# Optimization experiments

Hardware: AMD Instinct MI355X
Metric: run time of the kernel (lower is better)

The kernel has to match this reference:

```python
import jax, jax.numpy as jnp
import numpy as np

B, T_MAX, H, O, M, F = 256, 512, 512, 128, 512, 256


def setup_inputs() -> dict:
    key = jax.random.key(0)
    ks = jax.random.split(key, 20)
    s = 0.05
    n = lambda k, shape: (jax.random.normal(k, shape, dtype=jnp.float32) * s)
    features = jax.random.normal(ks[0], (B, F), dtype=jnp.float32)
    # PackedSequence-style: lengths sorted descending
    lengths = jnp.sort(jax.random.randint(ks[1], (B,), 1, T_MAX + 1))[::-1].astype(jnp.int32)
    return {
        'features': features,
        'lengths': lengths,
        'W_f2h': n(ks[2], (2 * H, F)), 'b_f2h': n(ks[3], (2 * H,)),
        'W_ih': n(ks[4], (4 * H, O)), 'W_hh': n(ks[5], (4 * H, H)),
        'b_ih': n(ks[6], (4 * H,)), 'b_hh': n(ks[7], (4 * H,)),
        'p1_W1': n(ks[8], (M, H)), 'p1_b1': n(ks[9], (M,)),
        'p1_W2': n(ks[10], (O, M)), 'p1_b2': n(ks[11], (O,)),
        'p2_W1': n(ks[12], (M, H)), 'p2_b1': n(ks[13], (M,)),
        'p2_W2': n(ks[14], (O, M)), 'p2_b2': n(ks[15], (O,)),
        'oW1': n(ks[16], (M, H)), 'ob1': n(ks[17], (M,)),
        'oW2': n(ks[18], (1, M)), 'ob2': n(ks[19], (1,)),
    }


def _mlp(x, W1, b1, W2, b2):
    return jnp.tanh(x @ W1.T + b1) @ W2.T + b2


def _packed_indices(lengths_np):
    T = int(lengths_np.max())
    bs = (lengths_np[None, :] > np.arange(T)[:, None]).sum(1)  # shrinking batch sizes
    t_idx = np.repeat(np.arange(T), bs)
    b_idx = np.concatenate([np.arange(n) for n in bs])
    return T, t_idx, b_idx


def reference(features, lengths, W_f2h, b_f2h, W_ih, W_hh, b_ih, b_hh,
              p1_W1, p1_b1, p1_W2, p1_b2, p2_W1, p2_b1, p2_W2, p2_b2,
              oW1, ob1, oW2, ob2):
    T, t_idx, b_idx = _packed_indices(np.asarray(lengths))

    # feature2hidden + view(-1, H, 2) split into (h, c)
    hc = (features @ W_f2h.T + b_f2h).reshape(-1, H, 2)
    h0, c0 = hc[..., 0], hc[..., 1]

    def step(carry, _):
        x, h, c = carry
        gates = x @ W_ih.T + b_ih + h @ W_hh.T + b_hh  # [B, 4H]
        i, f, g, o = jnp.split(gates, 4, axis=-1)
        c = jax.nn.sigmoid(f) * c + jax.nn.sigmoid(i) * jnp.tanh(g)
        h = jax.nn.sigmoid(o) * jnp.tanh(c)
        p1 = _mlp(h, p1_W1, p1_b1, p1_W2, p1_b2)
        p2 = _mlp(h, p2_W1, p2_b1, p2_W2, p2_b2)
        # emission_sampler in mean mode: next input = param1
        return (p1, h, c), (h, p1, p2)

    x0 = jnp.zeros((features.shape[0], O), dtype=features.dtype)
    _, (hs, p1s, p2s) = jax.lax.scan(step, (x0, h0, c0), None, length=T)

    # gather packed (flattened) outputs; rows >= batch_size[t] are never emitted,
    # matching the torch shrinking-batch loop exactly
    rnn_flat = hs[t_idx, b_idx]
    p1_flat = p1s[t_idx, b_idx]
    p2_flat = p2s[t_idx, b_idx]
    out_flat = p1_flat  # batched_input = emission_sampler(p1, p2) = p1
    offset_flat = _mlp(rnn_flat, oW1, ob1, oW2, ob2)[..., 0]
    return ((p1_flat, p2_flat), offset_flat, out_flat)
```

## Files before the change

kernel.cpp:

```cpp
#include <hip/hip_runtime.h>
#include <hip/hip_bf16.h>


#define NBLK 256
#define NTHR 512
#define ACT_STRIDE 2096

typedef __attribute__((ext_vector_type(8))) short bf16x8;
typedef __attribute__((ext_vector_type(4))) float f32x4;
typedef __hip_bfloat16 bf16;
typedef unsigned long long u64;

#define WS_BAR     0ull
#define WS_BS      32768ull
#define WS_OFF     34816ull
#define WS_BIASQ0  36864ull
#define WS_BIASQF  45056ull
#define WS_BCAT    53248ull
#define WS_B2CAT   59392ull
#define WS_C0      61440ull
#define WS_H       585728ull
#define WS_ACAT    1110016ull
#define WS_WQF     2682880ull
#define WS_W1T     6877184ull
#define WS_W2T     8450048ull

#define LDSG_OFF   67072
#define DYN_LDS    84480

__device__ __forceinline__ float sigm(float x) { return 1.0f / (1.0f + __expf(-x)); }
__device__ __forceinline__ unsigned short f2bu(float x) {
  bf16 b = __float2bfloat16(x);
  return *(unsigned short*)&b;
}
__device__ __forceinline__ u64 ld8a(const void* p) {
  return __hip_atomic_load((const u64*)p, __ATOMIC_RELAXED, __HIP_MEMORY_SCOPE_AGENT);
}
__device__ __forceinline__ bf16x8 ld16a(const short* p) {
  union { u64 u[2]; bf16x8 v; } t;
  t.u[0] = ld8a(p);
  t.u[1] = ld8a(p + 4);
  return t.v;
}
__device__ __forceinline__ void st4c(short* p, unsigned v) {
  __hip_atomic_store((unsigned*)p, v, __ATOMIC_RELAXED, __HIP_MEMORY_SCOPE_AGENT);
}
__device__ __forceinline__ bf16x8 actA(const char* smem, int row, int k0) {
  return *(const bf16x8*)(smem + row * ACT_STRIDE + k0 * 2);
}

__global__ void k_fold(char* ws, const float* __restrict__ Wih, const float* __restrict__ Whh,
                       const float* __restrict__ bih, const float* __restrict__ bhh,
                       const float* __restrict__ p1W2, const float* __restrict__ p1b2) {
  const int q = blockIdx.x;
  const int j = q >> 2, g = q & 3;
  const int orig = g * 512 + j;
  __shared__ float wih[128];
  if (threadIdx.x < 128) wih[threadIdx.x] = Wih[orig * 128 + threadIdx.x];
  __syncthreads();
  bf16* Wq = (bf16*)(ws + WS_WQF);
  for (int k = threadIdx.x; k < 512; k += 256)
    Wq[(size_t)q * 1024 + k] = __float2bfloat16(Whh[orig * 512 + k]);
  for (int m = threadIdx.x; m < 512; m += 256) {
    float s = 0.f;
    for (int o = 0; o < 128; ++o) s += wih[o] * p1W2[o * 512 + m];
    Wq[(size_t)q * 1024 + 512 + m] = __float2bfloat16(s);
  }
  if (threadIdx.x == 0) {
    float b0 = bih[orig] + bhh[orig];
    ((float*)(ws + WS_BIASQ0))[q] = b0;
    float s = 0.f;
    for (int o = 0; o < 128; ++o) s += wih[o] * p1b2[o];
    ((float*)(ws + WS_BIASQF))[q] = b0 + s;
  }
}

__global__ void k_w1t(char* ws, const float* w1a, const float* b1a, const float* w1b,
                      const float* b1b, const float* w1c, const float* b1c) {
  const int r = blockIdx.x;
  const int m = r & 511;
  const float* src = (r < 512) ? w1a : ((r < 1024) ? w1b : w1c);
  const float* bsrc = (r < 512) ? b1a : ((r < 1024) ? b1b : b1c);
  bf16* W = (bf16*)(ws + WS_W1T);
  const int c16 = r >> 4, l15 = r & 15;
  for (int k = threadIdx.x; k < 512; k += 256) {
    const int kk = k >> 5, l16 = (k >> 3) & 3, jj = k & 7;
    const size_t dst = ((((size_t)c16 * 16 + kk) * 16 + l15) * 4 + l16) * 8 + jj;
    W[dst] = __float2bfloat16(src[m * 512 + k]);
  }
  if (threadIdx.x == 0) ((float*)(ws + WS_BCAT))[r] = bsrc[m];
}

__global__ void k_w2t(char* ws, const float* w2a, const float* b2a, const float* w2b,
                      const float* b2b, const float* w2c, const float* b2c) {
  const int r = blockIdx.x;
  bf16* W = (bf16*)(ws + WS_W2T);
  float* bb = (float*)(ws + WS_B2CAT);
  const float* src = nullptr; const float* bsrc = nullptr; int m = 0;
  if (r < 128)      { src = w2a; bsrc = b2a; m = r; }
  else if (r < 256) { src = w2b; bsrc = b2b; m = r - 128; }
  else if (r == 256){ src = w2c; bsrc = b2c; m = 0; }
  const int t16 = r >> 4, l15 = r & 15;
  for (int k = threadIdx.x; k < 512; k += 256) {
    const int kk = k >> 5, l16 = (k >> 3) & 3, jj = k & 7;
    const size_t dst = ((((size_t)t16 * 16 + kk) * 16 + l15) * 4 + l16) * 8 + jj;
    W[dst] = src ? __float2bfloat16(src[m * 512 + k]) : __float2bfloat16(0.f);
  }
  if (threadIdx.x == 0) bb[r] = src ? bsrc[m] : 0.f;
}

__global__ void k_h0c0(char* ws, const float* __restrict__ features,
                       const float* __restrict__ Wf2h, const float* __restrict__ bf2h_) {
  const int r = blockIdx.x;
  __shared__ float feat[256];
  feat[threadIdx.x] = features[r * 256 + threadIdx.x];
  __syncthreads();
  float* C0 = (float*)(ws + WS_C0);
  bf16* H0 = (bf16*)(ws + WS_H);
  for (int n = threadIdx.x; n < 1024; n += 256) {
    float s = bf2h_[n];
    for (int k = 0; k < 256; ++k) s += Wf2h[n * 256 + k] * feat[k];
    const int j = n >> 1;
    if (n & 1) C0[r * 512 + j] = s;
    else       H0[(size_t)r * 512 + j] = __float2bfloat16(s);
  }
}

__global__ void k_bs(char* ws, const int* __restrict__ lengths) {
  __shared__ int sl[256];
  __shared__ int sbs[512];
  const int t = threadIdx.x;
  if (t < 256) sl[t] = lengths[t];
  __syncthreads();
  int c = 0;
  for (int b = 0; b < 256; ++b) c += (sl[b] > t) ? 1 : 0;
  sbs[t] = c;
  ((int*)(ws + WS_BS))[t] = c;
  __syncthreads();
  int o = 0;
  for (int u = 0; u < t; ++u) o += sbs[u];
  ((int*)(ws + WS_OFF))[t] = o;
}

__device__ __forceinline__ void stage_tile(char* smem, const short* gsrc, int rowstride,
                                           int R0, int ofs, int tid) {
  u64 v[8];
#pragma unroll
  for (int it = 0; it < 8; ++it) {
    const int c = tid + it * 512;
    const int row = c >> 7, cc = c & 127;
    v[it] = ld8a(gsrc + (size_t)(R0 + row) * rowstride + cc * 4);
  }
#pragma unroll
  for (int it = 0; it < 8; ++it) {
    const int c = tid + it * 512;
    const int row = c >> 7, cc = c & 127;
    *(u64*)(smem + row * ACT_STRIDE + ofs + cc * 8) = v[it];
  }
}

__device__ __forceinline__ void do_outs(int tm1, const short* __restrict__ Acur, int R0,
                                        int rt2, int l15, int l16, int tile,
                                        const short* __restrict__ W2T, const float* __restrict__ b2cat,
                                        const int* __restrict__ bsarr, const int* __restrict__ offarr,
                                        float* __restrict__ out, int N) {
  const int kb = tile < 8 ? 0 : (tile < 16 ? 512 : 1024);
  const short* ar = Acur + (size_t)(R0 + rt2 * 16 + l15) * 1536 + kb + l16 * 8;
  f32x4 acc = {0.f, 0.f, 0.f, 0.f};
#pragma unroll
  for (int kk = 0; kk < 16; ++kk) {
    bf16x8 av = ld16a(ar + kk * 32);
    bf16x8 bv = *(const bf16x8*)(W2T + ((((size_t)tile * 16 + kk) * 16 + l15) * 4 + l16) * 8);
    acc = __builtin_amdgcn_mfma_f32_16x16x32_bf16(av, bv, acc, 0, 0, 0);
  }
  const int wrow = tile * 16 + l15;
  const float bb = b2cat[wrow];
  const int bsz = bsarr[tm1], base = offarr[tm1];
  const int col = wrow;
  float* out_p1 = out;
  float* out_p2 = out + (size_t)N * 128;
  float* out_of = out + (size_t)N * 256;
  float* out_xx = out + (size_t)N * 257;
#pragma unroll
  for (int r = 0; r < 4; ++r) {
    const int R = R0 + rt2 * 16 + l16 * 4 + r;
    if (R < bsz) {
      const float v = acc[r] + bb;
      const size_t orow = (size_t)(base + R);
      if (col < 128)      { out_p1[orow * 128 + col] = v; out_xx[orow * 128 + col] = v; }
      else if (col < 256) { out_p2[orow * 128 + col - 128] = v; }
      else if (l15 == 0)  { out_of[orow] = v; }
    }
  }
}

__global__ void __launch_bounds__(NTHR) scan_kernel(char* ws, const int* __restrict__ lengths,
                                                    float* __restrict__ out, int N) {
  extern __shared__ char smem[];
  float* ldsg = (float*)(smem + LDSG_OFF);

  const int bid = blockIdx.x, tid = threadIdx.x;
  const int grp = bid >> 5, lb = bid & 31;
  const int R0 = grp * 32;
  const int wave = tid >> 6, lane = tid & 63;
  const int l15 = lane & 15, l16 = lane >> 4;

  unsigned* barG = (unsigned*)(ws + WS_BAR) + grp * 1024;
  const int* bsarr = (const int*)(ws + WS_BS);
  const int* offarr = (const int*)(ws + WS_OFF);
  const float* biasq0 = (const float*)(ws + WS_BIASQ0);
  const float* biasqF = (const float*)(ws + WS_BIASQF);
  const float* bcat = (const float*)(ws + WS_BCAT);
  const float* b2cat = (const float*)(ws + WS_B2CAT);
  const float* C0 = (const float*)(ws + WS_C0);
  short* Hb = (short*)(ws + WS_H);
  short* Ab = (short*)(ws + WS_ACAT);
  const short* WQF = (const short*)(ws + WS_WQF);
  const short* W1T = (const short*)(ws + WS_W1T);
  const short* W2T = (const short*)(ws + WS_W2T);

  const int ct = wave & 3, khalf = wave >> 2;
  const int qb = lb * 64;
  const int ct3 = (wave < 6) ? (wave % 3) : 0;
  const int rt3 = (wave < 6) ? (wave / 3) : 0;
  const int cb = lb * 48 + ct3 * 16;

  stage_tile(smem, Hb, 512, R0, 0, tid);

  bf16x8 bfrA[16];
#pragma unroll
  for (int kk = 0; kk < 16; ++kk)
    bfrA[kk] = *(const bf16x8*)(WQF + (size_t)(qb + ct * 16 + l15) * 1024 +
                                khalf * 512 + kk * 32 + l16 * 8);
  bf16x8 bfrB[16];
  if (wave < 6) {
    const int cb16 = lb * 3 + ct3;
#pragma unroll
    for (int kk = 0; kk < 16; ++kk)
      bfrB[kk] = *(const bf16x8*)(W1T + ((((size_t)cb16 * 16 + kk) * 16 + l15) * 4 + l16) * 8);
  }
  const float bbB = (wave < 6) ? bcat[cb + l15] : 0.f;

  const int Lr = tid >> 4, lj = tid & 15;
  float c_reg = C0[(R0 + Lr) * 512 + lb * 16 + lj];
  float b0_[4], bF_[4];
#pragma unroll
  for (int g = 0; g < 4; ++g) {
    const int q = qb + lj * 4 + g;
    b0_[g] = biasq0[q];
    bF_[g] = biasqF[q];
  }
  const int Lg = lengths[R0];
  __syncthreads();

  for (int t = 0; t < Lg; ++t) {
    const int par = t & 1, parn = par ^ 1;

    f32x4 acc0 = {0.f, 0.f, 0.f, 0.f}, acc1 = {0.f, 0.f, 0.f, 0.f};
    if (!(t == 0 && khalf == 1)) {
#pragma unroll
      for (int kk = 0; kk < 16; ++kk) {
        const int k0 = khalf * 512 + kk * 32 + l16 * 8;
        bf16x8 a0 = actA(smem, l15, k0);
        bf16x8 a1v = actA(smem, 16 + l15, k0);
        acc0 = __builtin_amdgcn_mfma_f32_16x16x32_bf16(a0, bfrA[kk], acc0, 0, 0, 0);
        acc1 = __builtin_amdgcn_mfma_f32_16x16x32_bf16(a1v, bfrA[kk], acc1, 0, 0, 0);
      }
    }
    {
      float* lg = ldsg + khalf * 2176;
#pragma unroll
      for (int r = 0; r < 4; ++r) {
        lg[(l16 * 4 + r) * 68 + ct * 16 + l15] = acc0[r];
        lg[(16 + l16 * 4 + r) * 68 + ct * 16 + l15] = acc1[r];
      }
    }
    __syncthreads();

    {
      const float* g0 = ldsg + Lr * 68 + lj * 4;
      const float* g1 = ldsg + 2176 + Lr * 68 + lj * 4;
      const float gi = g0[0] + g1[0] + (t ? bF_[0] : b0_[0]);
      const float gf = g0[1] + g1[1] + (t ? bF_[1] : b0_[1]);
      const float gg = g0[2] + g1[2] + (t ? bF_[2] : b0_[2]);
      const float go = g0[3] + g1[3] + (t ? bF_[3] : b0_[3]);
      c_reg = sigm(gf) * c_reg + sigm(gi) * tanhf(gg);
      const float h = sigm(go) * tanhf(c_reg);
      const float hp = __shfl_xor(h, 1);
      if ((lj & 1) == 0) {
        const unsigned v = (unsigned)f2bu(h) | ((unsigned)f2bu(hp) << 16);
        st4c(Hb + parn * (256 * 512) + (size_t)(R0 + Lr) * 512 + lb * 16 + lj, v);
      }
    }

    __syncthreads();
    if (tid == 0) {
      __hip_atomic_fetch_add(&barG[t * 2], 1u, __ATOMIC_RELAXED, __HIP_MEMORY_SCOPE_AGENT);
      while (__hip_atomic_load(&barG[t * 2], __ATOMIC_RELAXED, __HIP_MEMORY_SCOPE_AGENT) < 32u)
        __builtin_amdgcn_s_sleep(1);
    }
    __syncthreads();

    stage_tile(smem, Hb + parn * (256 * 512), 512, R0, 0, tid);
    __syncthreads();

    if (wave < 6) {
      f32x4 a3 = {0.f, 0.f, 0.f, 0.f};
#pragma unroll
      for (int kk = 0; kk < 16; ++kk) {
        bf16x8 av = actA(smem, rt3 * 16 + l15, kk * 32 + l16 * 8);
        a3 = __builtin_amdgcn_mfma_f32_16x16x32_bf16(av, bfrB[kk], a3, 0, 0, 0);
      }
      short* aout = Ab + parn * (256 * 1536);
#pragma unroll
      for (int r = 0; r < 4; ++r) {
        const float v = tanhf(a3[r] + bbB);
        const float vp = __shfl_xor(v, 1);
        if ((l15 & 1) == 0) {
          const unsigned pv = (unsigned)f2bu(v) | ((unsigned)f2bu(vp) << 16);
          st4c(aout + (size_t)(R0 + rt3 * 16 + l16 * 4 + r) * 1536 + cb + l15, pv);
        }
      }
    } else if (t > 0 && lb < 17) {
      do_outs(t - 1, Ab + par * (256 * 1536), R0, wave - 6, l15, l16, lb, W2T, b2cat,
              bsarr, offarr, out, N);
    }

    __syncthreads();
    if (tid == 0) {
      __hip_atomic_fetch_add(&barG[t * 2 + 1], 1u, __ATOMIC_RELAXED, __HIP_MEMORY_SCOPE_AGENT);
      while (__hip_atomic_load(&barG[t * 2 + 1], __ATOMIC_RELAXED, __HIP_MEMORY_SCOPE_AGENT) < 32u)
        __builtin_amdgcn_s_sleep(1);
    }
    __syncthreads();

    stage_tile(smem, Ab + parn * (256 * 1536), 1536, R0, 1024, tid);
    __syncthreads();
  }

  if (lb < 17 && wave >= 6)
    do_outs(Lg - 1, Ab + (Lg & 1) * (256 * 1536), R0, wave - 6, l15, l16, lb, W2T, b2cat,
            bsarr, offarr, out, N);
}

extern "C" void kernel_launch(void* const* d_in, const int* in_sizes, int n_in,
                              void* d_out, int out_size, void* d_ws, size_t ws_size,
                              hipStream_t stream) {
  const float* features = (const float*)d_in[0];
  const int* lengths = (const int*)d_in[1];
  const float* Wf2h = (const float*)d_in[2];
  const float* bf2h_ = (const float*)d_in[3];
  const float* Wih = (const float*)d_in[4];
  const float* Whh = (const float*)d_in[5];
  const float* bih = (const float*)d_in[6];
  const float* bhh = (const float*)d_in[7];
  const float* p1W1 = (const float*)d_in[8];
  const float* p1b1 = (const float*)d_in[9];
  const float* p1W2 = (const float*)d_in[10];
  const float* p1b2 = (const float*)d_in[11];
  const float* p2W1 = (const float*)d_in[12];
  const float* p2b1 = (const float*)d_in[13];
  const float* p2W2 = (const float*)d_in[14];
  const float* p2b2 = (const float*)d_in[15];
  const float* oW1 = (const float*)d_in[16];
  const float* ob1 = (const float*)d_in[17];
  const float* oW2 = (const float*)d_in[18];
  const float* ob2 = (const float*)d_in[19];

  char* ws = (char*)d_ws;
  float* outp = (float*)d_out;
  int N = out_size / 385;

  hipMemsetAsync(ws + WS_BAR, 0, 32768, stream);
  k_fold<<<2048, 256, 0, stream>>>(ws, Wih, Whh, bih, bhh, p1W2, p1b2);
  k_w1t<<<1536, 256, 0, stream>>>(ws, p1W1, p1b1, p2W1, p2b1, oW1, ob1);
  k_w2t<<<272, 256, 0, stream>>>(ws, p1W2, p1b2, p2W2, p2b2, oW2, ob2);
  k_h0c0<<<256, 256, 0, stream>>>(ws, features, Wf2h, bf2h_);
  k_bs<<<1, 512, 0, stream>>>(ws, lengths);

  hipFuncSetAttribute((const void*)scan_kernel,
                      hipFuncAttributeMaxDynamicSharedMemorySize, DYN_LDS);

  const int* lenv = lengths;
  void* args[] = {&ws, &lenv, &outp, &N};
  hipLaunchCooperativeKernel((const void*)scan_kernel, dim3(NBLK), dim3(NTHR),
                             args, DYN_LDS, stream);
}
```

Baseline: 6.227 ms.

## Restructure LSTM scan step to overlap MLP hidden layer with recurrent GEMM

Reorganizes each time step so the recurrent h·W_hh part of the gates and the MLP hidden-layer GEMM (h·W1, tanh) run concurrently on different waves from the same staged h tile. The folded p1-input contribution is then computed after a grid barrier from the freshly staged A tile. This removes one serial phase from the per-step critical path. The output projection (do_outs) now runs between the barrier arrive and wait, so it is overlapped with the barrier latency. Barrier counters double in size and an epilogue step handles the final hidden layer, adding extra complexity around the barrier indexing.

```diff
diff --git a/kernel.cpp b/kernel.cpp
--- a/kernel.cpp
+++ b/kernel.cpp
@@ -12,18 +12,18 @@
 typedef unsigned long long u64;
 
 #define WS_BAR     0ull
-#define WS_BS      32768ull
-#define WS_OFF     34816ull
-#define WS_BIASQ0  36864ull
-#define WS_BIASQF  45056ull
-#define WS_BCAT    53248ull
-#define WS_B2CAT   59392ull
-#define WS_C0      61440ull
-#define WS_H       585728ull
-#define WS_ACAT    1110016ull
-#define WS_WQF     2682880ull
-#define WS_W1T     6877184ull
-#define WS_W2T     8450048ull
+#define WS_BS      65536ull
+#define WS_OFF     67584ull
+#define WS_BIASQ0  69632ull
+#define WS_BIASQF  77824ull
+#define WS_BCAT    86016ull
+#define WS_B2CAT   92160ull
+#define WS_C0      94208ull
+#define WS_H       618496ull
+#define WS_ACAT    1142784ull
+#define WS_WQF     2715648ull
+#define WS_W1T     6909952ull
+#define WS_W2T     8482816ull
 
 #define LDSG_OFF   67072
 #define DYN_LDS    84480
@@ -32,6 +32,9 @@
 __device__ __forceinline__ unsigned short f2bu(float x) {
   bf16 b = __float2bfloat16(x);
   return *(unsigned short*)&b;
+}
+__device__ __forceinline__ unsigned packbf(float v, float vp) {
+  return (unsigned)f2bu(v) | ((unsigned)f2bu(vp) << 16);
 }
 __device__ __forceinline__ u64 ld8a(const void* p) {
   return __hip_atomic_load((const u64*)p, __ATOMIC_RELAXED, __HIP_MEMORY_SCOPE_AGENT);
@@ -44,9 +47,6 @@
 }
 __device__ __forceinline__ void st4c(short* p, unsigned v) {
   __hip_atomic_store((unsigned*)p, v, __ATOMIC_RELAXED, __HIP_MEMORY_SCOPE_AGENT);
-}
-__device__ __forceinline__ bf16x8 actA(const char* smem, int row, int k0) {
-  return *(const bf16x8*)(smem + row * ACT_STRIDE + k0 * 2);
 }
 
 __global__ void k_fold(char* ws, const float* __restrict__ Wih, const float* __restrict__ Whh,
@@ -159,6 +159,50 @@
   }
 }
 
+__device__ __forceinline__ void ph1_acat(const char* smem, short* AbW, int R0, int lb,
+                                         int wave, int l15, int l16,
+                                         const bf16x8* bfrP, float bbP) {
+  if (wave < 2) {
+    f32x4 a3 = {0.f, 0.f, 0.f, 0.f};
+#pragma unroll
+    for (int kk = 0; kk < 16; ++kk) {
+      bf16x8 av = *(const bf16x8*)(smem + (wave * 16 + l15) * ACT_STRIDE +
+                                   (kk * 32 + l16 * 8) * 2);
+      a3 = __builtin_amdgcn_mfma_f32_16x16x32_bf16(av, bfrP[kk], a3, 0, 0, 0);
+    }
+#pragma unroll
+    for (int r = 0; r < 4; ++r) {
+      const float v = tanhf(a3[r] + bbP);
+      const float vp = __shfl_xor(v, 1);
+      if ((l15 & 1) == 0)
+        st4c(AbW + (size_t)(R0 + wave * 16 + l16 * 4 + r) * 1536 + lb * 16 + l15,
+             packbf(v, vp));
+    }
+  } else if (wave >= 6) {
+    const int cbase = (wave == 6 ? 512 : 1024) + lb * 16;
+    f32x4 acc0 = {0.f, 0.f, 0.f, 0.f}, acc1 = {0.f, 0.f, 0.f, 0.f};
+#pragma unroll
+    for (int kk = 0; kk < 16; ++kk) {
+      const int k0b = (kk * 32 + l16 * 8) * 2;
+      bf16x8 a0 = *(const bf16x8*)(smem + l15 * ACT_STRIDE + k0b);
+      bf16x8 a1v = *(const bf16x8*)(smem + (16 + l15) * ACT_STRIDE + k0b);
+      acc0 = __builtin_amdgcn_mfma_f32_16x16x32_bf16(a0, bfrP[kk], acc0, 0, 0, 0);
+      acc1 = __builtin_amdgcn_mfma_f32_16x16x32_bf16(a1v, bfrP[kk], acc1, 0, 0, 0);
+    }
+#pragma unroll
+    for (int r = 0; r < 4; ++r) {
+      const float v = tanhf(acc0[r] + bbP);
+      const float vp = __shfl_xor(v, 1);
+      if ((l15 & 1) == 0)
+        st4c(AbW + (size_t)(R0 + l16 * 4 + r) * 1536 + cbase + l15, packbf(v, vp));
+      const float w = tanhf(acc1[r] + bbP);
+      const float wp = __shfl_xor(w, 1);
+      if ((l15 & 1) == 0)
+        st4c(AbW + (size_t)(R0 + 16 + l16 * 4 + r) * 1536 + cbase + l15, packbf(w, wp));
+    }
+  }
+}
+
 __device__ __forceinline__ void do_outs(int tm1, const short* __restrict__ Acur, int R0,
                                         int rt2, int l15, int l16, int tile,
                                         const short* __restrict__ W2T, const float* __restrict__ b2cat,
@@ -205,7 +249,7 @@
   const int wave = tid >> 6, lane = tid & 63;
   const int l15 = lane & 15, l16 = lane >> 4;
 
-  unsigned* barG = (unsigned*)(ws + WS_BAR) + grp * 1024;
+  unsigned* barG = (unsigned*)(ws + WS_BAR) + grp * 2048;
   const int* bsarr = (const int*)(ws + WS_BS);
   const int* offarr = (const int*)(ws + WS_OFF);
   const float* biasq0 = (const float*)(ws + WS_BIASQ0);
@@ -219,27 +263,31 @@
   const short* W1T = (const short*)(ws + WS_W1T);
   const short* W2T = (const short*)(ws + WS_W2T);
 
-  const int ct = wave & 3, khalf = wave >> 2;
   const int qb = lb * 64;
-  const int ct3 = (wave < 6) ? (wave % 3) : 0;
-  const int rt3 = (wave < 6) ? (wave / 3) : 0;
-  const int cb = lb * 48 + ct3 * 16;
+  const int ctF = wave & 3, rtF = wave >> 2;
 
   stage_tile(smem, Hb, 512, R0, 0, tid);
 
-  bf16x8 bfrA[16];
+  bf16x8 bfrF[16];
 #pragma unroll
   for (int kk = 0; kk < 16; ++kk)
-    bfrA[kk] = *(const bf16x8*)(WQF + (size_t)(qb + ct * 16 + l15) * 1024 +
-                                khalf * 512 + kk * 32 + l16 * 8);
-  bf16x8 bfrB[16];
-  if (wave < 6) {
-    const int cb16 = lb * 3 + ct3;
+    bfrF[kk] = *(const bf16x8*)(WQF + (size_t)(qb + ctF * 16 + l15) * 1024 +
+                                512 + kk * 32 + l16 * 8);
+  bf16x8 bfrP[16];
+  float bbP = 0.f;
+  if (wave >= 2 && wave < 6) {
+    const int ct = wave - 2;
 #pragma unroll
     for (int kk = 0; kk < 16; ++kk)
-      bfrB[kk] = *(const bf16x8*)(W1T + ((((size_t)cb16 * 16 + kk) * 16 + l15) * 4 + l16) * 8);
-  }
-  const float bbB = (wave < 6) ? bcat[cb + l15] : 0.f;
+      bfrP[kk] = *(const bf16x8*)(WQF + (size_t)(qb + ct * 16 + l15) * 1024 +
+                                  kk * 32 + l16 * 8);
+  } else {
+    const int c16p = (wave < 2) ? lb : (wave == 6 ? 32 + lb : 64 + lb);
+#pragma unroll
+    for (int kk = 0; kk < 16; ++kk)
+      bfrP[kk] = *(const bf16x8*)(W1T + ((((size_t)c16p * 16 + kk) * 16 + l15) * 4 + l16) * 8);
+    bbP = bcat[c16p * 16 + l15];
+  }
 
   const int Lr = tid >> 4, lj = tid & 15;
   float c_reg = C0[(R0 + Lr) * 512 + lb * 16 + lj];
@@ -255,25 +303,52 @@
 
   for (int t = 0; t < Lg; ++t) {
     const int par = t & 1, parn = par ^ 1;
-
-    f32x4 acc0 = {0.f, 0.f, 0.f, 0.f}, acc1 = {0.f, 0.f, 0.f, 0.f};
-    if (!(t == 0 && khalf == 1)) {
+    short* AbW = Ab + parn * (256 * 1536);
+
+    if (wave >= 2 && wave < 6) {
+      const int ct = wave - 2;
+      f32x4 acc0 = {0.f, 0.f, 0.f, 0.f}, acc1 = {0.f, 0.f, 0.f, 0.f};
 #pragma unroll
       for (int kk = 0; kk < 16; ++kk) {
-        const int k0 = khalf * 512 + kk * 32 + l16 * 8;
-        bf16x8 a0 = actA(smem, l15, k0);
-        bf16x8 a1v = actA(smem, 16 + l15, k0);
-        acc0 = __builtin_amdgcn_mfma_f32_16x16x32_bf16(a0, bfrA[kk], acc0, 0, 0, 0);
-        acc1 = __builtin_amdgcn_mfma_f32_16x16x32_bf16(a1v, bfrA[kk], acc1, 0, 0, 0);
+        const int k0b = (kk * 32 + l16 * 8) * 2;
+        bf16x8 a0 = *(const bf16x8*)(smem + l15 * ACT_STRIDE + k0b);
+        bf16x8 a1v = *(const bf16x8*)(smem + (16 + l15) * ACT_STRIDE + k0b);
+        acc0 = __builtin_amdgcn_mfma_f32_16x16x32_bf16(a0, bfrP[kk], acc0, 0, 0, 0);
+        acc1 = __builtin_amdgcn_mfma_f32_16x16x32_bf16(a1v, bfrP[kk], acc1, 0, 0, 0);
       }
-    }
+#pragma unroll
+      for (int r = 0; r < 4; ++r) {
+        ldsg[(l16 * 4 + r) * 68 + ct * 16 + l15] = acc0[r];
+        ldsg[(16 + l16 * 4 + r) * 68 + ct * 16 + l15] = acc1[r];
+      }
+    } else {
+      ph1_acat(smem, AbW, R0, lb, wave, l15, l16, bfrP, bbP);
+    }
+    __syncthreads();
+
+    if (tid == 0) {
+      __hip_atomic_fetch_add(&barG[t * 2], 1u, __ATOMIC_RELAXED, __HIP_MEMORY_SCOPE_AGENT);
+      while (__hip_atomic_load(&barG[t * 2], __ATOMIC_RELAXED, __HIP_MEMORY_SCOPE_AGENT) < 32u)
+        __builtin_amdgcn_s_sleep(1);
+    }
+    __syncthreads();
+
+    stage_tile(smem, AbW, 1536, R0, 1024, tid);
+    __syncthreads();
+
     {
-      float* lg = ldsg + khalf * 2176;
-#pragma unroll
-      for (int r = 0; r < 4; ++r) {
-        lg[(l16 * 4 + r) * 68 + ct * 16 + l15] = acc0[r];
-        lg[(16 + l16 * 4 + r) * 68 + ct * 16 + l15] = acc1[r];
+      f32x4 accF = {0.f, 0.f, 0.f, 0.f};
+      if (t > 0) {
+#pragma unroll
+        for (int kk = 0; kk < 16; ++kk) {
+          bf16x8 av = *(const bf16x8*)(smem + (rtF * 16 + l15) * ACT_STRIDE + 1024 +
+                                       (kk * 32 + l16 * 8) * 2);
+          accF = __builtin_amdgcn_mfma_f32_16x16x32_bf16(av, bfrF[kk], accF, 0, 0, 0);
+        }
       }
+#pragma unroll
+      for (int r = 0; r < 4; ++r)
+        ldsg[2176 + (rtF * 16 + l16 * 4 + r) * 68 + ctF * 16 + l15] = accF[r];
     }
     __syncthreads();
 
@@ -288,59 +363,41 @@
       const float h = sigm(go) * tanhf(c_reg);
       const float hp = __shfl_xor(h, 1);
       if ((lj & 1) == 0) {
-        const unsigned v = (unsigned)f2bu(h) | ((unsigned)f2bu(hp) << 16);
+        const unsigned v = packbf(h, hp);
         st4c(Hb + parn * (256 * 512) + (size_t)(R0 + Lr) * 512 + lb * 16 + lj, v);
       }
     }
-
-    __syncthreads();
+    __syncthreads();
+
+    if (tid == 0)
+      __hip_atomic_fetch_add(&barG[t * 2 + 1], 1u, __ATOMIC_RELAXED, __HIP_MEMORY_SCOPE_AGENT);
+    if (t > 0 && lb < 17 && wave >= 6)
+      do_outs(t - 1, AbW, R0, wave - 6, l15, l16, lb, W2T, b2cat, bsarr, offarr, out, N);
     if (tid == 0) {
-      __hip_atomic_fetch_add(&barG[t * 2], 1u, __ATOMIC_RELAXED, __HIP_MEMORY_SCOPE_AGENT);
-      while (__hip_atomic_load(&barG[t * 2], __ATOMIC_RELAXED, __HIP_MEMORY_SCOPE_AGENT) < 32u)
-        __builtin_amdgcn_s_sleep(1);
-    }
-    __syncthreads();
-
-    stage_tile(smem, Hb + parn * (256 * 512), 512, R0, 0, tid);
-    __syncthreads();
-
-    if (wave < 6) {
-      f32x4 a3 = {0.f, 0.f, 0.f, 0.f};
-#pragma unroll
-      for (int kk = 0; kk < 16; ++kk) {
-        bf16x8 av = actA(smem, rt3 * 16 + l15, kk * 32 + l16 * 8);
-        a3 = __builtin_amdgcn_mfma_f32_16x16x32_bf16(av, bfrB[kk], a3, 0, 0, 0);
-      }
-      short* aout = Ab + parn * (256 * 1536);
-#pragma unroll
-      for (int r = 0; r < 4; ++r) {
-        const float v = tanhf(a3[r] + bbB);
-        const float vp = __shfl_xor(v, 1);
-        if ((l15 & 1) == 0) {
-          const unsigned pv = (unsigned)f2bu(v) | ((unsigned)f2bu(vp) << 16);
-          st4c(aout + (size_t)(R0 + rt3 * 16 + l16 * 4 + r) * 1536 + cb + l15, pv);
-        }
-      }
-    } else if (t > 0 && lb < 17) {
-      do_outs(t - 1, Ab + par * (256 * 1536), R0, wave - 6, l15, l16, lb, W2T, b2cat,
-              bsarr, offarr, out, N);
-    }
-
-    __syncthreads();
-    if (tid == 0) {
-      __hip_atomic_fetch_add(&barG[t * 2 + 1], 1u, __ATOMIC_RELAXED, __HIP_MEMORY_SCOPE_AGENT);
       while (__hip_atomic_load(&barG[t * 2 + 1], __ATOMIC_RELAXED, __HIP_MEMORY_SCOPE_AGENT) < 32u)
         __builtin_amdgcn_s_sleep(1);
     }
     __syncthreads();
 
-    stage_tile(smem, Ab + parn * (256 * 1536), 1536, R0, 1024, tid);
-    __syncthreads();
-  }
-
-  if (lb < 17 && wave >= 6)
-    do_outs(Lg - 1, Ab + (Lg & 1) * (256 * 1536), R0, wave - 6, l15, l16, lb, W2T, b2cat,
-            bsarr, offarr, out, N);
+    stage_tile(smem, Hb + parn * (256 * 512), 512, R0, 0, tid);
+    __syncthreads();
+  }
+
+  {
+    const int parE = (Lg & 1) ^ 1;
+    short* AbW = Ab + parE * (256 * 1536);
+    if (!(wave >= 2 && wave < 6))
+      ph1_acat(smem, AbW, R0, lb, wave, l15, l16, bfrP, bbP);
+    __syncthreads();
+    if (tid == 0) {
+      __hip_atomic_fetch_add(&barG[2 * Lg], 1u, __ATOMIC_RELAXED, __HIP_MEMORY_SCOPE_AGENT);
+      while (__hip_atomic_load(&barG[2 * Lg], __ATOMIC_RELAXED, __HIP_MEMORY_SCOPE_AGENT) < 32u)
+        __builtin_amdgcn_s_sleep(1);
+    }
+    __syncthreads();
+    if (lb < 17 && wave >= 6)
+      do_outs(Lg - 1, AbW, R0, wave - 6, l15, l16, lb, W2T, b2cat, bsarr, offarr, out, N);
+  }
 }
 
 extern "C" void kernel_launch(void* const* d_in, const int* in_sizes, int n_in,
@@ -371,7 +428,7 @@
   float* outp = (float*)d_out;
   int N = out_size / 385;
 
-  hipMemsetAsync(ws + WS_BAR, 0, 32768, stream);
+  hipMemsetAsync(ws + WS_BAR, 0, 65536, stream);
   k_fold<<<2048, 256, 0, stream>>>(ws, Wih, Whh, bih, bhh, p1W2, p1b2);
   k_w1t<<<1536, 256, 0, stream>>>(ws, p1W1, p1b1, p2W1, p2b1, oW1, ob1);
   k_w2t<<<272, 256, 0, stream>>>(ws, p1W2, p1b2, p2W2, p2b2, oW2, ob2);
```

Result: slower. 7.090 ms (+13.9%).
